# Kernel tuning notes

Hardware: AMD Instinct MI355X
Metric: run time of the kernel (lower is better)

Reference implementation:

```python
import jax, jax.numpy as jnp
import numpy as np
import math

N_TOTAL = 262144
C = 128
B = 512
LMAX = 512  # max segment length (static for jit)


def setup_inputs() -> dict:
    key = jax.random.key(0)
    ks = jax.random.split(key, 8)
    Q_feature = jax.random.normal(ks[0], (N_TOTAL, C), dtype=jnp.float32)
    K_feature = jax.random.normal(ks[1], (N_TOTAL, C), dtype=jnp.float32)
    # cumulative offsets: equal segments of length LMAX (general code handles ragged)
    offset = (jnp.arange(1, B + 1, dtype=jnp.int64) * (N_TOTAL // B))
    s = 1.0 / math.sqrt(C)
    Wq = jax.random.normal(ks[2], (C, C), dtype=jnp.float32) * s
    Wk = jax.random.normal(ks[3], (C, C), dtype=jnp.float32) * s
    Wv = jax.random.normal(ks[4], (C, C), dtype=jnp.float32) * s
    bq = jnp.zeros((C,), dtype=jnp.float32)
    bk = jnp.zeros((C,), dtype=jnp.float32)
    bv = jnp.zeros((C,), dtype=jnp.float32)
    return {"Q_feature": Q_feature, "K_feature": K_feature,
            "Wq": Wq, "bq": bq, "Wk": Wk, "bk": bk, "Wv": Wv, "bv": bv,
            "offset": offset}


def reference(Q_feature, K_feature, Wq, bq, Wk, bk, Wv, bv, offset):
    N, Cdim = Q_feature.shape
    Q = Q_feature @ Wq.T + bq
    K = K_feature @ Wk.T + bk
    V = K_feature @ Wv.T + bv

    starts = jnp.concatenate([jnp.zeros((1,), offset.dtype), offset[:-1]])
    lengths = offset - starts                         # (B,)
    pos = jnp.arange(LMAX)                            # (LMAX,)
    idx = jnp.clip(starts[:, None] + pos[None, :], 0, N - 1)  # (B, LMAX)
    mask = pos[None, :] < lengths[:, None]            # (B, LMAX) valid tokens

    Qp = Q[idx]                                       # (B, LMAX, C)
    Kp = K[idx]
    Vp = V[idx]

    scale = 1.0 / math.sqrt(Cdim)
    scores = jnp.einsum('blc,bmc->blm', Qp, Kp) * scale     # (B, LMAX, LMAX)
    scores = jnp.where(mask[:, None, :], scores, jnp.float32(-1e30))
    attn = jax.nn.softmax(scores, axis=-1)
    outp = jnp.einsum('blm,bmc->blc', attn, Vp)             # (B, LMAX, C)
    outp = outp * mask[:, :, None]                          # zero padded rows

    # scatter padded segments back to flat (N, C); idx is an exact partition on valid rows
    out = jnp.zeros((N, Cdim), dtype=outp.dtype).at[idx].add(outp)
    return out
```

## Files before the change

### kernel.cpp

```cpp
#include <hip/hip_runtime.h>
#include <hip/hip_bf16.h>

#define CDIM 128
#define LMAXC 512
#define QBLK 128
#define KVBLK 64

#define QSCALE (0.08838834764831845f * 1.4426950408889634f)

typedef __attribute__((ext_vector_type(8))) short bf16x8;
typedef __attribute__((ext_vector_type(4))) short bf16x4;
typedef __attribute__((ext_vector_type(4))) float f32x4;

__device__ inline short f2bf(float f) {
    union { float f; unsigned u; } v; v.f = f;
    unsigned r = v.u + 0x7FFFu + ((v.u >> 16) & 1u);
    return (short)(r >> 16);
}

__device__ inline bf16x8 cvt8v(float4 a, float4 b) {
    bf16x8 o;
    o[0] = f2bf(a.x); o[1] = f2bf(a.y); o[2] = f2bf(a.z); o[3] = f2bf(a.w);
    o[4] = f2bf(b.x); o[5] = f2bf(b.y); o[6] = f2bf(b.z); o[7] = f2bf(b.w);
    return o;
}

__device__ inline unsigned pk2(float lo, float hi) {
    unsigned r;
    asm("v_cvt_pk_bf16_f32 %0, %1, %2" : "=v"(r) : "v"(lo), "v"(hi));
    return r;
}

__device__ inline void gload16(const void* g, void* l) {
    __builtin_amdgcn_global_load_lds(
        (const __attribute__((address_space(1))) unsigned*)g,
        (__attribute__((address_space(3))) unsigned*)l, 16, 0, 0);
}

__device__ inline void blk_barrier() {
    __builtin_amdgcn_sched_barrier(0);
    __builtin_amdgcn_s_barrier();
    __builtin_amdgcn_sched_barrier(0);
}

__device__ inline int pch(int q) { return ((q + (q >> 3)) & 7) << 4; }

__global__ void wcvt_kernel(const float* __restrict__ Wq,
                            const float* __restrict__ Wk,
                            const float* __restrict__ Wv,
                            short* __restrict__ Wbf)
{
    int t = blockIdx.x * 256 + threadIdx.x;
    int m = t / 2048;
    int e = (t % 2048) * 8;
    const float* W = (m == 0) ? Wq : (m == 1) ? Wk : Wv;
    float sc = (m == 0) ? QSCALE : 1.0f;
    float4 a = *reinterpret_cast<const float4*>(W + e);
    float4 b = *reinterpret_cast<const float4*>(W + e + 4);
    a.x *= sc; a.y *= sc; a.z *= sc; a.w *= sc;
    b.x *= sc; b.y *= sc; b.z *= sc; b.w *= sc;
    *reinterpret_cast<bf16x8*>(Wbf + m * 16384 + e) = cvt8v(a, b);
}

__global__ __launch_bounds__(256, 4) void proj_kernel(
    const float* __restrict__ Qf, const float* __restrict__ Kf,
    const short* __restrict__ Wbf,
    const float* __restrict__ bq, const float* __restrict__ bk,
    const float* __restrict__ bv,
    short* __restrict__ Qp, short* __restrict__ Kp, short* __restrict__ Vt,
    int N)
{
    __shared__ __align__(16) char vt_lds[16384];

    const int tid   = threadIdx.x;
    const int lane  = tid & 63;
    const int wv    = tid >> 6;
    const int lrow  = lane & 15;
    const int lhalf = lane >> 4;
    const int row0  = blockIdx.x * 128;
    const bool isQ  = (blockIdx.y == 0);
    const float* X  = isQ ? Qf : Kf;

    bf16x8 xfr[2][4];
#pragma unroll
    for (int xt = 0; xt < 2; ++xt) {
        const float* xr = X + (size_t)(row0 + wv * 32 + xt * 16 + lrow) * CDIM;
#pragma unroll
        for (int ks = 0; ks < 4; ++ks) {
            const float4* s = reinterpret_cast<const float4*>(xr + ks * 32 + lhalf * 8);
            xfr[xt][ks] = cvt8v(s[0], s[1]);
        }
    }

    {
        const short* W    = isQ ? Wbf : Wbf + 16384;
        const float* bias = isQ ? bq : bk;
        const float  bsc  = isQ ? QSCALE : 1.0f;
        short* outp       = isQ ? Qp : Kp;

#pragma unroll
        for (int cf = 0; cf < 8; ++cf) {
            const short* wr = W + (cf * 16 + lrow) * CDIM;
            bf16x8 wfr[4];
#pragma unroll
            for (int ks = 0; ks < 4; ++ks)
                wfr[ks] = *reinterpret_cast<const bf16x8*>(wr + ks * 32 + lhalf * 8);
            float4 bv4 = *reinterpret_cast<const float4*>(bias + cf * 16 + lhalf * 4);
#pragma unroll
            for (int xt = 0; xt < 2; ++xt) {
                f32x4 acc = {0.f, 0.f, 0.f, 0.f};
#pragma unroll
                for (int ks = 0; ks < 4; ++ks)
                    acc = __builtin_amdgcn_mfma_f32_16x16x32_bf16(wfr[ks], xfr[xt][ks], acc, 0, 0, 0);
                bf16x4 pk;
                pk[0] = f2bf(acc[0] + bv4.x * bsc);
                pk[1] = f2bf(acc[1] + bv4.y * bsc);
                pk[2] = f2bf(acc[2] + bv4.z * bsc);
                pk[3] = f2bf(acc[3] + bv4.w * bsc);
                *reinterpret_cast<bf16x4*>(
                    outp + (size_t)(row0 + wv * 32 + xt * 16 + lrow) * CDIM
                         + cf * 16 + lhalf * 4) = pk;
            }
        }
    }

    if (!isQ) {
        const short* W = Wbf + 32768;
#pragma unroll
        for (int ph = 0; ph < 2; ++ph) {
#pragma unroll
            for (int c4 = 0; c4 < 4; ++c4) {
                const int cf = ph * 4 + c4;
                f32x4 acc0 = {0.f, 0.f, 0.f, 0.f};
                f32x4 acc1 = {0.f, 0.f, 0.f, 0.f};
                const short* wr = W + (cf * 16 + lrow) * CDIM;
#pragma unroll
                for (int ks = 0; ks < 4; ++ks) {
                    bf16x8 bfr = *reinterpret_cast<const bf16x8*>(wr + ks * 32 + lhalf * 8);
                    acc0 = __builtin_amdgcn_mfma_f32_16x16x32_bf16(xfr[0][ks], bfr, acc0, 0, 0, 0);
                    acc1 = __builtin_amdgcn_mfma_f32_16x16x32_bf16(xfr[1][ks], bfr, acc1, 0, 0, 0);
                }
                const int colL = c4 * 16 + lrow;
                float bcol = bv[ph * 64 + colL];
                bf16x4 p0, p1;
#pragma unroll
                for (int r = 0; r < 4; ++r) {
                    p0[r] = f2bf(acc0[r] + bcol);
                    p1[r] = f2bf(acc1[r] + bcol);
                }
                int base = colL * 256 + wv * 64 + lhalf * 8;
                int sw   = (colL & 7) << 4;
                *reinterpret_cast<bf16x4*>(vt_lds + ((base)      ^ sw)) = p0;
                *reinterpret_cast<bf16x4*>(vt_lds + ((base + 32) ^ sw)) = p1;
            }
            __syncthreads();
#pragma unroll
            for (int it = 0; it < 4; ++it) {
                int c    = it * 256 + tid;
                int colL = c >> 4, rc = c & 15;
                int a    = (colL * 256 + rc * 16) ^ ((colL & 7) << 4);
                bf16x8 v = *reinterpret_cast<const bf16x8*>(vt_lds + a);
                *reinterpret_cast<bf16x8*>(
                    Vt + (size_t)(ph * 64 + colL) * N + row0 + rc * 8) = v;
            }
            __syncthreads();
        }
    }
}

__global__ __launch_bounds__(256) void attn_kernel(
    const short* __restrict__ Qp, const short* __restrict__ Kp,
    const short* __restrict__ VtG, const int* __restrict__ offset,
    float* __restrict__ out, int Ntot)
{
    __shared__ __align__(16) char smem[81920];
    char* lds_p = smem + 65536;

    const int nq = LMAXC / QBLK;
    int flat = blockIdx.x, total = gridDim.x;
    int seg, qb;
    if ((total & (8 * nq - 1)) == 0) {
        int per = total >> 3;
        int xcd = flat & 7;
        int wi  = flat >> 3;
        int sl  = wi / nq;
        qb  = wi - sl * nq;
        seg = xcd * (per / nq) + sl;
    } else { seg = flat / nq; qb = flat - seg * nq; }

    const int start = (seg == 0) ? 0 : offset[seg - 1];
    int len = offset[seg] - start;
    if (len > LMAXC) len = LMAXC;
    const int q0 = qb * QBLK;
    if (q0 >= len) return;

    const int tid   = threadIdx.x;
    const int lane  = tid & 63;
    const int wv    = tid >> 6;
    const int lrow  = lane & 15;
    const int lhalf = lane >> 4;
    const int ntiles = (len + KVBLK - 1) / KVBLK;
    const int lm1 = len - 1;

    auto stage = [&](int kv0, int bb) {
        char* kb = smem + bb * 32768;
        char* vb = kb + 16384;
#pragma unroll
        for (int j = 0; j < 4; ++j) {
            int beta = j * 4096 + wv * 1024 + (lane << 4);
            int r  = beta >> 8;
            int gs = ((beta >> 4) & 15) ^ (r & 7);
            int rg = kv0 + r; if (rg > lm1) rg = lm1;
            gload16(Kp + (((size_t)(start + rg)) << 7) + (gs << 3),
                    kb + j * 4096 + wv * 1024);
            int d   = beta >> 7;
            int gs2 = ((beta >> 4) & 7) ^ (d & 7);
            long gk = (long)start + kv0 + (gs2 << 3);
            if (gk + 8 > Ntot) gk = Ntot - 8;
            gload16(VtG + (size_t)d * Ntot + gk,
                    vb + j * 4096 + wv * 1024);
        }
    };

    stage(0, 0);

    bf16x8 aq[2][4];
#pragma unroll
    for (int qt = 0; qt < 2; ++qt) {
        int qr = q0 + wv * 32 + qt * 16 + lrow;
        if (qr > lm1) qr = lm1;
        const short* qrow = Qp + (size_t)(start + qr) * CDIM;
#pragma unroll
        for (int ks = 0; ks < 4; ++ks)
            aq[qt][ks] = *reinterpret_cast<const bf16x8*>(qrow + ks * 32 + lhalf * 8);
    }

    f32x4 acc_o[2][8];
    float lsum[2] = {0.f, 0.f};
#pragma unroll
    for (int qt = 0; qt < 2; ++qt)
#pragma unroll
        for (int df = 0; df < 8; ++df) acc_o[qt][df] = (f32x4){0.f, 0.f, 0.f, 0.f};

    const int wbase = wv * 4096;

    for (int t = 0; t < ntiles; ++t) {
        const int kv0 = t * KVBLK;
        const int bb  = t & 1;
        if (t + 1 < ntiles) {
            stage(kv0 + KVBLK, bb ^ 1);
            asm volatile("s_waitcnt vmcnt(8)" ::: "memory");
        } else {
            asm volatile("s_waitcnt vmcnt(0)" ::: "memory");
        }
        blk_barrier();

        char* lds_k  = smem + bb * 32768;
        char* lds_vt = lds_k + 16384;
        const bool tail = (kv0 + KVBLK > len);

        f32x4 s0[4], s1[4];
        __builtin_amdgcn_s_setprio(1);
#pragma unroll
        for (int kf = 0; kf < 4; ++kf) {
            s0[kf] = (f32x4){0.f, 0.f, 0.f, 0.f};
            s1[kf] = (f32x4){0.f, 0.f, 0.f, 0.f};
            int key = kf * 16 + lrow;
#pragma unroll
            for (int ks = 0; ks < 4; ++ks) {
                int kbo = (key * 256 + (ks * 32 + lhalf * 8) * 2) ^ ((key & 7) << 4);
                bf16x8 kfr = *reinterpret_cast<const bf16x8*>(lds_k + kbo);
                s0[kf] = __builtin_amdgcn_mfma_f32_16x16x32_bf16(kfr, aq[0][ks], s0[kf], 0, 0, 0);
                s1[kf] = __builtin_amdgcn_mfma_f32_16x16x32_bf16(kfr, aq[1][ks], s1[kf], 0, 0, 0);
            }
        }
        __builtin_amdgcn_s_setprio(0);

        const int keyb0 = kv0 + lhalf * 4;
#pragma unroll
        for (int qt = 0; qt < 2; ++qt) {
            const int qlocal = qt * 16 + lrow;
            const int rowoff = wbase + qlocal * 128;
            const int swz = pch(qlocal);
#pragma unroll
            for (int kf = 0; kf < 4; ++kf) {
                f32x4 sv = qt ? s1[kf] : s0[kf];
                float p[4];
#pragma unroll
                for (int r = 0; r < 4; ++r) {
                    float pv = exp2f(sv[r]);
                    if (tail && (keyb0 + kf * 16 + r >= len)) pv = 0.f;
                    p[r] = pv;
                    lsum[qt] += pv;
                }
                unsigned long long w =
                    (unsigned long long)pk2(p[0], p[1]) |
                    ((unsigned long long)pk2(p[2], p[3]) << 32);
                *reinterpret_cast<unsigned long long*>(
                    lds_p + rowoff + ((kf * 32 + lhalf * 8) ^ swz)) = w;
            }
        }

        __builtin_amdgcn_s_setprio(1);
#pragma unroll
        for (int ks2 = 0; ks2 < 2; ++ks2) {
            bf16x8 ap0 = *reinterpret_cast<const bf16x8*>(
                lds_p + wbase + lrow * 128 + ((ks2 * 64 + lhalf * 16) ^ pch(lrow)));
            bf16x8 ap1 = *reinterpret_cast<const bf16x8*>(
                lds_p + wbase + (16 + lrow) * 128 + ((ks2 * 64 + lhalf * 16) ^ pch(16 + lrow)));
            int k0 = ks2 * 32 + lhalf * 8;
#pragma unroll
            for (int df = 0; df < 8; ++df) {
                int d = df * 16 + lrow;
                int vb2 = (d * 128 + k0 * 2) ^ ((d & 7) << 4);
                bf16x8 bvf = *reinterpret_cast<const bf16x8*>(lds_vt + vb2);
                acc_o[0][df] = __builtin_amdgcn_mfma_f32_16x16x32_bf16(ap0, bvf, acc_o[0][df], 0, 0, 0);
                acc_o[1][df] = __builtin_amdgcn_mfma_f32_16x16x32_bf16(ap1, bvf, acc_o[1][df], 0, 0, 0);
            }
        }
        __builtin_amdgcn_s_setprio(0);

        blk_barrier();
    }

#pragma unroll
    for (int qt = 0; qt < 2; ++qt) {
        float l = lsum[qt];
        l += __shfl_xor(l, 16);
        l += __shfl_xor(l, 32);
        float rinv[4];
#pragma unroll
        for (int r = 0; r < 4; ++r)
            rinv[r] = 1.0f / __shfl(l, lhalf * 4 + r);
#pragma unroll
        for (int df = 0; df < 8; ++df)
#pragma unroll
            for (int r = 0; r < 4; ++r) {
                int qg = q0 + wv * 32 + qt * 16 + lhalf * 4 + r;
                if (qg < len)
                    out[(size_t)(start + qg) * CDIM + df * 16 + lrow]
                        = acc_o[qt][df][r] * rinv[r];
            }
    }
}

extern "C" void kernel_launch(void* const* d_in, const int* in_sizes, int n_in,
                              void* d_out, int out_size, void* d_ws, size_t ws_size,
                              hipStream_t stream) {
    const float* Qf = (const float*)d_in[0];
    const float* Kf = (const float*)d_in[1];
    const float* Wq = (const float*)d_in[2];
    const float* bq = (const float*)d_in[3];
    const float* Wk = (const float*)d_in[4];
    const float* bk = (const float*)d_in[5];
    const float* Wv = (const float*)d_in[6];
    const float* bv_ = (const float*)d_in[7];
    const int* offset = (const int*)d_in[8];

    const int N = in_sizes[0] / CDIM;
    const int B = in_sizes[8];

    short* Qp = (short*)d_ws;
    short* Kp = Qp + (size_t)N * CDIM;
    short* Vt = Kp + (size_t)N * CDIM;
    float* out = (float*)d_out;

    size_t base_need = (size_t)3 * N * CDIM * 2;
    short* Wbf = (ws_size >= base_need + 3 * 16384 * 2)
               ? (Vt + (size_t)N * CDIM) : (short*)d_out;

    wcvt_kernel<<<24, 256, 0, stream>>>(Wq, Wk, Wv, Wbf);

    dim3 pgrid(N / 128, 2);
    proj_kernel<<<pgrid, 256, 0, stream>>>(Qf, Kf, Wbf, bq, bk, bv_,
                                           Qp, Kp, Vt, N);

    attn_kernel<<<dim3(B * (LMAXC / QBLK)), 256, 0, stream>>>(
        Qp, Kp, Vt, offset, out, N);
}
```

Measured before the change: 285.3 us.

## Split V projection into its own grid slice and stage weights in LDS

The projection grid grows from two to three y-slices, so Q, K and V projections each get their own block instead of K blocks also computing V. Each block first copies its 128x128 bf16 weight matrix into a swizzled LDS buffer and reads MFMA weight fragments from there instead of global memory. This balances the work across blocks and cuts repeated global weight loads. The cost is that K_feature is now read and converted twice, LDS per block grows to 48KB, and the occupancy hint in the launch bounds is dropped, which may lower occupancy.

```diff
diff --git a/kernel.cpp b/kernel.cpp
--- a/kernel.cpp
+++ b/kernel.cpp
@@ -62,7 +62,7 @@
     *reinterpret_cast<bf16x8*>(Wbf + m * 16384 + e) = cvt8v(a, b);
 }
 
-__global__ __launch_bounds__(256, 4) void proj_kernel(
+__global__ __launch_bounds__(256) void proj_kernel(
     const float* __restrict__ Qf, const float* __restrict__ Kf,
     const short* __restrict__ Wbf,
     const float* __restrict__ bq, const float* __restrict__ bk,
@@ -70,7 +70,9 @@
     short* __restrict__ Qp, short* __restrict__ Kp, short* __restrict__ Vt,
     int N)
 {
-    __shared__ __align__(16) char vt_lds[16384];
+    __shared__ __align__(16) char lds[49152];
+    char* wlds   = lds;
+    char* vt_lds = lds + 32768;
 
     const int tid   = threadIdx.x;
     const int lane  = tid & 63;
@@ -78,8 +80,17 @@
     const int lrow  = lane & 15;
     const int lhalf = lane >> 4;
     const int row0  = blockIdx.x * 128;
-    const bool isQ  = (blockIdx.y == 0);
-    const float* X  = isQ ? Qf : Kf;
+    const int which = blockIdx.y;
+    const float* X  = (which == 0) ? Qf : Kf;
+    const short* Wg = Wbf + which * 16384;
+
+#pragma unroll
+    for (int j = 0; j < 8; ++j) {
+        int beta = j * 4096 + tid * 16;
+        int r  = beta >> 8;
+        int gs = ((beta >> 4) & 15) ^ (r & 7);
+        gload16(Wg + r * 128 + gs * 8, wlds + beta);
+    }
 
     bf16x8 xfr[2][4];
 #pragma unroll
@@ -91,20 +102,22 @@
             xfr[xt][ks] = cvt8v(s[0], s[1]);
         }
     }
-
-    {
-        const short* W    = isQ ? Wbf : Wbf + 16384;
-        const float* bias = isQ ? bq : bk;
-        const float  bsc  = isQ ? QSCALE : 1.0f;
-        short* outp       = isQ ? Qp : Kp;
+    __syncthreads();
+
+    if (which < 2) {
+        const float* bias = (which == 0) ? bq : bk;
+        const float  bsc  = (which == 0) ? QSCALE : 1.0f;
+        short* outp       = (which == 0) ? Qp : Kp;
 
 #pragma unroll
         for (int cf = 0; cf < 8; ++cf) {
-            const short* wr = W + (cf * 16 + lrow) * CDIM;
+            const int key = cf * 16 + lrow;
             bf16x8 wfr[4];
 #pragma unroll
-            for (int ks = 0; ks < 4; ++ks)
-                wfr[ks] = *reinterpret_cast<const bf16x8*>(wr + ks * 32 + lhalf * 8);
+            for (int ks = 0; ks < 4; ++ks) {
+                int wb = (key * 256 + (ks * 32 + lhalf * 8) * 2) ^ ((key & 7) << 4);
+                wfr[ks] = *reinterpret_cast<const bf16x8*>(wlds + wb);
+            }
             float4 bv4 = *reinterpret_cast<const float4*>(bias + cf * 16 + lhalf * 4);
 #pragma unroll
             for (int xt = 0; xt < 2; ++xt) {
@@ -122,32 +135,35 @@
                          + cf * 16 + lhalf * 4) = pk;
             }
         }
-    }
-
-    if (!isQ) {
-        const short* W = Wbf + 32768;
+    } else {
 #pragma unroll
         for (int ph = 0; ph < 2; ++ph) {
 #pragma unroll
             for (int c4 = 0; c4 < 4; ++c4) {
-                const int cf = ph * 4 + c4;
+                const int cf  = ph * 4 + c4;
+                const int key = cf * 16 + lrow;
+                bf16x8 wfr[4];
+#pragma unroll
+                for (int ks = 0; ks < 4; ++ks) {
+                    int wb = (key * 256 + (ks * 32 + lhalf * 8) * 2) ^ ((key & 7) << 4);
+                    wfr[ks] = *reinterpret_cast<const bf16x8*>(wlds + wb);
+                }
                 f32x4 acc0 = {0.f, 0.f, 0.f, 0.f};
                 f32x4 acc1 = {0.f, 0.f, 0.f, 0.f};
-                const short* wr = W + (cf * 16 + lrow) * CDIM;
 #pragma unroll
                 for (int ks = 0; ks < 4; ++ks) {
-                    bf16x8 bfr = *reinterpret_cast<const bf16x8*>(wr + ks * 32 + lhalf * 8);
-                    acc0 = __builtin_amdgcn_mfma_f32_16x16x32_bf16(xfr[0][ks], bfr, acc0, 0, 0, 0);
-                    acc1 = __builtin_amdgcn_mfma_f32_16x16x32_bf16(xfr[1][ks], bfr, acc1, 0, 0, 0);
+                    acc0 = __builtin_amdgcn_mfma_f32_16x16x32_bf16(xfr[0][ks], wfr[ks], acc0, 0, 0, 0);
+                    acc1 = __builtin_amdgcn_mfma_f32_16x16x32_bf16(xfr[1][ks], wfr[ks], acc1, 0, 0, 0);
                 }
-                const int colL = c4 * 16 + lrow;
-                float bcol = bv[ph * 64 + colL];
+                const int col = cf * 16 + lrow;
+                float bcol = bv[col];
                 bf16x4 p0, p1;
 #pragma unroll
                 for (int r = 0; r < 4; ++r) {
                     p0[r] = f2bf(acc0[r] + bcol);
                     p1[r] = f2bf(acc1[r] + bcol);
                 }
+                const int colL = c4 * 16 + lrow;
                 int base = colL * 256 + wv * 64 + lhalf * 8;
                 int sw   = (colL & 7) << 4;
                 *reinterpret_cast<bf16x4*>(vt_lds + ((base)      ^ sw)) = p0;
@@ -371,7 +387,7 @@
 
     wcvt_kernel<<<24, 256, 0, stream>>>(Wq, Wk, Wv, Wbf);
 
-    dim3 pgrid(N / 128, 2);
+    dim3 pgrid(N / 128, 3);
     proj_kernel<<<pgrid, 256, 0, stream>>>(Qf, Kf, Wbf, bq, bk, bv_,
                                            Qp, Kp, Vt, N);
 
```

Result: faster. 248.2 us (-13.0%).
